# Performance work log

Measured on AMD Instinct MI355X. Metric: run time of the kernel, lower is better.

Reference implementation:

```python
import jax, jax.numpy as jnp
import numpy as np

PRIMES = [2, 3, 5, 7]  # from prime2idx {"2":0,"3":1,"5":2,"7":3}
NEG = float('-inf')


def setup_inputs() -> dict:
    B, O, T, P, L = 16384, 7, 64, 4, 7
    ks = jax.random.split(jax.random.key(0), 12)
    return {
        'program_seq': jax.random.randint(ks[0], (B, 20), 0, 7),
        'order_mask': jnp.zeros((B, O), jnp.float32),
        'tile_remain_budgets': jax.random.randint(ks[1], (B, L, P), 0, T),
        'tile_masks': jnp.zeros((B, L, P, T), jnp.float32),
        'cur_buffer_level': 1,
        'loop_ind': 2,
        'remain_buffer_size': jax.random.uniform(ks[2], (B,), jnp.float32, 1.0, 1e6),
        'tile2_max': jax.random.randint(ks[3], (B,), 32, T),
        'max_temporal_tile2': jax.random.uniform(ks[4], (B,), jnp.float32, 0.0, 10.0),
        'sp_tile2_max': jax.random.randint(ks[5], (B,), 16, 32),
        'sp_tile2_min': jax.random.randint(ks[6], (B,), 0, 8),
        'order_logit': jax.random.normal(ks[7], (B, O), jnp.float32),
        'tile_logits': jax.random.normal(ks[8], (B, P, T), jnp.float32),
        'sp_tile2_logit': jax.random.normal(ks[9], (B, T), jnp.float32),
    }


def _sample(key, score, mask):
    # categorical sample, its log-prob, and the 'more-than-one-option' mask
    action = jax.random.categorical(key, score)
    lp = jnp.take_along_axis(jax.nn.log_softmax(score, axis=-1), action[:, None], axis=1)[:, 0]
    lpm = ((mask == 0).sum(axis=-1) > 1).astype(score.dtype)
    return action, lp, lpm


def reference(program_seq, order_mask, tile_remain_budgets, tile_masks,
              cur_buffer_level, loop_ind, remain_buffer_size, tile2_max,
              max_temporal_tile2, sp_tile2_max, sp_tile2_min,
              order_logit, tile_logits, sp_tile2_logit):
    B = program_seq.shape[0]
    T = tile_masks.shape[-1]
    P = tile_logits.shape[1]
    n_levels = 3  # len(buffer_size_list)
    keys = jax.random.split(jax.random.key(1), 2 + P)
    j = jnp.arange(T)[None, :]  # [1,T] position grid for range masks

    # ---- order head ----
    order_score = order_logit + order_mask
    order_action, order_lp, order_lpm = _sample(keys[0], order_score, order_mask)

    if cur_buffer_level == n_levels:
        log_probs = jnp.zeros((B, 1 + P + 1), order_score.dtype).at[:, 0].set(order_lp)
        log_prob_masks = jnp.zeros((B, 1 + P + 1), order_score.dtype).at[:, 0].set(order_lpm)
        return order_action, None, None, log_probs, log_prob_masks

    tile2_base = tile_masks[:, loop_ind, 0]  # [B,T]

    # ---- spatial tile2: vectorized [min,max] range mask (replaces per-sample loops) ----
    sp_mask = jnp.where((j > sp_tile2_max[:, None]) | (j < sp_tile2_min[:, None]), NEG, tile2_base)
    sp_score = sp_tile2_logit + sp_mask
    sp_action, sp_lp, sp_lpm = _sample(keys[1], sp_score, sp_mask)

    # ---- temporal tile2 ----
    tile2_min = sp_action
    t2_max = jnp.minimum(tile2_max, tile2_min + max_temporal_tile2.astype(tile2_max.dtype))
    t2_mask = jnp.where((j > t2_max[:, None]) | (j < tile2_min[:, None]), NEG, tile2_base)
    t2_score = tile_logits[:, 0] + t2_mask
    tile2_action, t2_lp, t2_lpm = _sample(keys[2], t2_score, t2_mask)

    tile_actions = [tile2_action]
    sp_tile_actions = [sp_action]
    log_probs = [order_lp, t2_lp]
    log_prob_masks = [order_lpm, t2_lpm]

    tile_action = tile2_action
    rbs = remain_buffer_size
    for p in range(1, P):  # small fixed loop over primes
        rbs = rbs / jnp.power(jnp.float32(PRIMES[p - 1]), tile_action.astype(jnp.float32))
        tmax = jnp.log2(jnp.clip(rbs, 1.0)) / np.log2(PRIMES[p])
        tmax = jnp.clip(tmax.astype(jnp.int32), 0, T - 1)
        tmax = jnp.minimum(tmax, tile_remain_budgets[:, loop_ind, p].astype(jnp.int32))
        mask = jnp.where(j > tmax[:, None], NEG, tile_masks[:, loop_ind, p])
        score = tile_logits[:, p] + mask
        tile_action, lp, lpm = _sample(keys[2 + p], score, mask)
        tile_actions.append(tile_action)
        log_probs.append(lp)
        log_prob_masks.append(lpm)
        sp_tile_actions.append(jnp.zeros((B,), program_seq.dtype))

    log_probs.append(sp_lp)
    log_prob_masks.append(sp_lpm)

    return (order_action,
            jnp.stack(tile_actions, axis=1),
            jnp.stack(sp_tile_actions, axis=1),
            jnp.stack(log_probs, axis=1),
            jnp.stack(log_prob_masks, axis=1))
```

## Files before the change

### kernel.cpp

```cpp
#include <hip/hip_runtime.h>
#include <stdint.h>
#include <math.h>

__host__ __device__ static inline void tf2x32(uint32_t k0, uint32_t k1,
                                              uint32_t& x0, uint32_t& x1) {
  uint32_t ks2 = k0 ^ k1 ^ 0x1BD11BDAu;
  x0 += k0; x1 += k1;
#define TFR(r) { x0 += x1; x1 = (x1 << (r)) | (x1 >> (32 - (r))); x1 ^= x0; }
  TFR(13) TFR(15) TFR(26) TFR(6)
  x0 += k1;  x1 += ks2 + 1u;
  TFR(17) TFR(29) TFR(16) TFR(24)
  x0 += ks2; x1 += k0 + 2u;
  TFR(13) TFR(15) TFR(26) TFR(6)
  x0 += k0;  x1 += k1 + 3u;
  TFR(17) TFR(29) TFR(16) TFR(24)
  x0 += k1;  x1 += ks2 + 4u;
  TFR(13) TFR(15) TFR(26) TFR(6)
  x0 += ks2; x1 += k0 + 5u;
#undef TFR
}

struct Keys { uint32_t k[12]; };

struct SampleOut { int action; float lp; float lpm; };

template <int CTRL>
__device__ __forceinline__ float dpp_max_step(float v) {
  int o = __builtin_amdgcn_update_dpp(__float_as_int(v), __float_as_int(v),
                                      CTRL, 0xf, 0xf, false);
  return fmaxf(v, __int_as_float(o));
}
template <int CTRL>
__device__ __forceinline__ float dpp_add_step(float v) {
  int o = __builtin_amdgcn_update_dpp(0, __float_as_int(v),
                                      CTRL, 0xf, 0xf, false);
  return v + __int_as_float(o);
}
__device__ __forceinline__ float wave_max_bcast(float v) {
  v = dpp_max_step<0x111>(v);
  v = dpp_max_step<0x112>(v);
  v = dpp_max_step<0x114>(v);
  v = dpp_max_step<0x118>(v);
  v = dpp_max_step<0x142>(v);
  v = dpp_max_step<0x143>(v);
  return __int_as_float(__builtin_amdgcn_readlane(__float_as_int(v), 63));
}
__device__ __forceinline__ float wave_sum_bcast(float v) {
  v = dpp_add_step<0x111>(v);
  v = dpp_add_step<0x112>(v);
  v = dpp_add_step<0x114>(v);
  v = dpp_add_step<0x118>(v);
  v = dpp_add_step<0x142>(v);
  v = dpp_add_step<0x143>(v);
  return __int_as_float(__builtin_amdgcn_readlane(__float_as_int(v), 63));
}

__device__ static inline SampleOut sample_pre(float z, float es, float sc_full,
                                              bool lpm_pred) {
  float zmax = wave_max_bcast(z);
  unsigned long long ball = __ballot(z == zmax);
  int action = __ffsll(ball) - 1;
  float essum = wave_sum_bcast(es);
  float sa = __int_as_float(
      __builtin_amdgcn_readlane(__float_as_int(sc_full), action));
  unsigned long long mb = __ballot(lpm_pred);
  SampleOut r;
  r.action = action;
  r.lp = sa - logf(essum);
  r.lpm = (__popcll(mb) > 1) ? 1.0f : 0.0f;
  return r;
}

__device__ static inline double ipow_d(int base, int e) {
  double r = 1.0, b = (double)base;
#pragma unroll
  for (int i = 0; i < 6; ++i) {
    if (e & (1 << i)) r *= b;
    b *= b;
  }
  return r;
}

__device__ static inline float gumbel_f(uint32_t k0, uint32_t k1,
                                        uint32_t flat_idx) {
  uint32_t x0 = 0u, x1 = flat_idx;
  tf2x32(k0, k1, x0, x1);
  uint32_t bits = x0 ^ x1;
  uint32_t fb = (bits >> 9) | 0x3f800000u;
  float f = __uint_as_float(fb) - 1.0f;
  const float tinyf = 1.1754943508222875e-38f;
  float u = fmaxf(tinyf, f + tinyf);
  return -logf(-logf(u));
}

__global__ __launch_bounds__(256) void pt_kernel(
    const int*   __restrict__ loop_ind_p,
    const float* __restrict__ order_mask,
    const int*   __restrict__ tile_remain_budgets,
    const float* __restrict__ tile_masks,
    const float* __restrict__ remain_buffer_size,
    const int*   __restrict__ tile2_max,
    const float* __restrict__ max_temporal_tile2,
    const int*   __restrict__ sp_tile2_max,
    const int*   __restrict__ sp_tile2_min,
    const float* __restrict__ order_logit,
    const float* __restrict__ tile_logits,
    const float* __restrict__ sp_tile2_logit,
    float*       __restrict__ out,
    int B, int O, int T, int P, int L, Keys keys) {
  const int wave = threadIdx.x >> 6;
  const int t    = threadIdx.x & 63;
  const int b    = blockIdx.x * (blockDim.x >> 6) + wave;
  if (b >= B) return;

  const float NEGINF = -__builtin_inff();
  const int li = loop_ind_p[0];

  float g0 = gumbel_f(keys.k[0],  keys.k[1],  (uint32_t)(b * O + t));
  uint32_t fT = (uint32_t)(b * T + t);
  float g1 = gumbel_f(keys.k[2],  keys.k[3],  fT);
  float g2 = gumbel_f(keys.k[4],  keys.k[5],  fT);
  float g3 = gumbel_f(keys.k[6],  keys.k[7],  fT);
  float g4 = gumbel_f(keys.k[8],  keys.k[9],  fT);
  float g5 = gumbel_f(keys.k[10], keys.k[11], fT);

  float om  = (t < O) ? order_mask[(size_t)b * O + t] : 1.0f;
  float osc = (t < O) ? (order_logit[(size_t)b * O + t] + om) : NEGINF;

  const float* tm_row = tile_masks + ((size_t)b * L + li) * P * T;
  const float* tl_row = tile_logits + (size_t)b * P * T;
  float base0 = tm_row[t];
  float base1 = tm_row[T + t];
  float base2 = tm_row[2 * T + t];
  float base3 = tm_row[3 * T + t];

  int spmx = sp_tile2_max[b], spmn = sp_tile2_min[b];
  float spmask = (t > spmx || t < spmn) ? NEGINF : base0;
  float spsc   = sp_tile2_logit[(size_t)b * T + t] + spmask;

  float sc2f = tl_row[t]         + base0;
  float sc3f = tl_row[T + t]     + base1;
  float sc4f = tl_row[2 * T + t] + base2;
  float sc5f = tl_row[3 * T + t] + base3;
  float es2f = expf(sc2f), es3f = expf(sc3f);
  float es4f = expf(sc4f), es5f = expf(sc5f);
  float z2f = sc2f + g2, z3f = sc3f + g3, z4f = sc4f + g4, z5f = sc5f + g5;

  const int* budg = tile_remain_budgets + ((size_t)b * L + li) * P;

  SampleOut so = sample_pre(osc + g0, expf(osc), osc,
                            (t < O) && (om == 0.0f));

  SampleOut ssp = sample_pre(spsc + g1, expf(spsc), spsc, spmask == 0.0f);

  int t2min = ssp.action;
  int mt = (int)max_temporal_tile2[b];
  int t2mx = min(tile2_max[b], t2min + mt);
  bool pv2 = (t <= t2mx) && (t >= t2min);
  SampleOut st2 = sample_pre(pv2 ? z2f : NEGINF, pv2 ? es2f : 0.0f, sc2f,
                             pv2 && (base0 == 0.0f));

  const float L2P1 = 1.5849625007211562f;
  const float L2P2 = 2.321928094887362f;
  const float L2P3 = 2.807354922057604f;

  float rbs = remain_buffer_size[b];
  int   pact[3];
  float plp[3], plpm[3];

  int prev = st2.action;
  {
    rbs = (float)((double)rbs / ipow_d(2, prev));
    double v = log2(fmax((double)rbs, 1.0)) / (double)L2P1;
    int tmax = min(T - 1, max(0, (int)v));
    tmax = min(tmax, budg[1]);
    bool pv = (t <= tmax);
    SampleOut s = sample_pre(pv ? z3f : NEGINF, pv ? es3f : 0.0f, sc3f,
                             pv && (base1 == 0.0f));
    pact[0] = s.action; plp[0] = s.lp; plpm[0] = s.lpm; prev = s.action;
  }
  {
    rbs = (float)((double)rbs / ipow_d(3, prev));
    double v = log2(fmax((double)rbs, 1.0)) / (double)L2P2;
    int tmax = min(T - 1, max(0, (int)v));
    tmax = min(tmax, budg[2]);
    bool pv = (t <= tmax);
    SampleOut s = sample_pre(pv ? z4f : NEGINF, pv ? es4f : 0.0f, sc4f,
                             pv && (base2 == 0.0f));
    pact[1] = s.action; plp[1] = s.lp; plpm[1] = s.lpm; prev = s.action;
  }
  {
    rbs = (float)((double)rbs / ipow_d(5, prev));
    double v = log2(fmax((double)rbs, 1.0)) / (double)L2P3;
    int tmax = min(T - 1, max(0, (int)v));
    tmax = min(tmax, budg[3]);
    bool pv = (t <= tmax);
    SampleOut s = sample_pre(pv ? z5f : NEGINF, pv ? es5f : 0.0f, sc5f,
                             pv && (base3 == 0.0f));
    pact[2] = s.action; plp[2] = s.lp; plpm[2] = s.lpm;
  }

  if (t == 0) {
    size_t Bz = (size_t)B;
    out[b] = (float)so.action;
    float* ta = out + Bz + (size_t)b * P;
    ta[0] = (float)st2.action;
    ta[1] = (float)pact[0]; ta[2] = (float)pact[1]; ta[3] = (float)pact[2];
    float* sa = out + Bz * (1 + P) + (size_t)b * P;
    sa[0] = (float)ssp.action; sa[1] = 0.0f; sa[2] = 0.0f; sa[3] = 0.0f;
    const int NL = 6;
    float* lp = out + Bz * (1 + 2 * P) + (size_t)b * NL;
    lp[0] = so.lp; lp[1] = st2.lp;
    lp[2] = plp[0]; lp[3] = plp[1]; lp[4] = plp[2];
    lp[5] = ssp.lp;
    float* lm = out + Bz * (1 + 2 * P + NL) + (size_t)b * NL;
    lm[0] = so.lpm; lm[1] = st2.lpm;
    lm[2] = plpm[0]; lm[3] = plpm[1]; lm[4] = plpm[2];
    lm[5] = ssp.lpm;
  }
}

extern "C" void kernel_launch(void* const* d_in, const int* in_sizes, int n_in,
                              void* d_out, int out_size, void* d_ws,
                              size_t ws_size, hipStream_t stream) {
  const int B = in_sizes[6];
  const int O = in_sizes[1] / B;
  const int T = in_sizes[13] / B;
  const int P = in_sizes[12] / (B * T);
  const int L = in_sizes[2] / (B * P);

  Keys keys;
  for (int j = 0; j < 6; ++j) {
    uint32_t x0 = 0u, x1 = (uint32_t)j;
    tf2x32(0u, 1u, x0, x1);
    keys.k[2 * j]     = x0;
    keys.k[2 * j + 1] = x1;
  }

  const int wavesPerBlock = 4;
  dim3 block(wavesPerBlock * 64);
  dim3 grid((B + wavesPerBlock - 1) / wavesPerBlock);
  pt_kernel<<<grid, block, 0, stream>>>(
      (const int*)d_in[5],
      (const float*)d_in[1],
      (const int*)d_in[2],
      (const float*)d_in[3],
      (const float*)d_in[6],
      (const int*)d_in[7],
      (const float*)d_in[8],
      (const int*)d_in[9],
      (const int*)d_in[10],
      (const float*)d_in[11],
      (const float*)d_in[12],
      (const float*)d_in[13],
      (float*)d_out, B, O, T, P, L, keys);
}
```

Baseline: 214.6 us.

## Replace double log2/pow chain with constant threshold tables and ballot counting

Replaces the serial double-precision power and log2 computation of each prime's tile bound with per-lane lookups into precomputed constant tables. Each lane holds one inverse power and one threshold, and the bound is obtained by ballot and popcount. Scalar loads are hoisted ahead of the sampling chain, the action index is made wave-uniform with readfirstlane, and the per-row output stores are vectorized. This shortens the latency-bound dependent chain per row, but threshold rounding must exactly match the reference's float/double log2 truncation.

```diff
diff --git a/kernel.cpp b/kernel.cpp
--- a/kernel.cpp
+++ b/kernel.cpp
@@ -24,6 +24,37 @@
 
 struct SampleOut { int action; float lp; float lpm; };
 
+struct DTab { double v[64]; };
+
+constexpr double CEXP2(double w) {
+  long i = (long)w;
+  double f = w - (double)i;
+  double y = f * 0.69314718055994530941723212145818;
+  double term = 1.0, sum = 1.0;
+  for (int k = 1; k <= 18; ++k) { term = term * y / (double)k; sum += term; }
+  double p = 1.0;
+  for (long k = 0; k < i; ++k) p *= 2.0;
+  return sum * p;
+}
+constexpr DTab make_thresh(double l2p) {
+  DTab t{};
+  t.v[0] = 1e300;
+  for (int k = 1; k < 64; ++k) t.v[k] = CEXP2((double)k * l2p);
+  return t;
+}
+constexpr DTab make_invpw(int p) {
+  DTab t{};
+  double pw = 1.0;
+  for (int k = 0; k < 64; ++k) { t.v[k] = 1.0 / pw; pw *= (double)p; }
+  return t;
+}
+__constant__ DTab THR3 = make_thresh((double)1.5849625007211562f);
+__constant__ DTab THR5 = make_thresh((double)2.321928094887362f);
+__constant__ DTab THR7 = make_thresh((double)2.807354922057604f);
+__constant__ DTab IPW2 = make_invpw(2);
+__constant__ DTab IPW3 = make_invpw(3);
+__constant__ DTab IPW5 = make_invpw(5);
+
 template <int CTRL>
 __device__ __forceinline__ float dpp_max_step(float v) {
   int o = __builtin_amdgcn_update_dpp(__float_as_int(v), __float_as_int(v),
@@ -55,11 +86,19 @@
   return __int_as_float(__builtin_amdgcn_readlane(__float_as_int(v), 63));
 }
 
+__device__ __forceinline__ double readlane_d(double v, int lane) {
+  union { double d; int i[2]; } u, r;
+  u.d = v;
+  r.i[0] = __builtin_amdgcn_readlane(u.i[0], lane);
+  r.i[1] = __builtin_amdgcn_readlane(u.i[1], lane);
+  return r.d;
+}
+
 __device__ static inline SampleOut sample_pre(float z, float es, float sc_full,
                                               bool lpm_pred) {
   float zmax = wave_max_bcast(z);
   unsigned long long ball = __ballot(z == zmax);
-  int action = __ffsll(ball) - 1;
+  int action = __builtin_amdgcn_readfirstlane(__ffsll(ball) - 1);
   float essum = wave_sum_bcast(es);
   float sa = __int_as_float(
       __builtin_amdgcn_readlane(__float_as_int(sc_full), action));
@@ -68,16 +107,6 @@
   r.action = action;
   r.lp = sa - logf(essum);
   r.lpm = (__popcll(mb) > 1) ? 1.0f : 0.0f;
-  return r;
-}
-
-__device__ static inline double ipow_d(int base, int e) {
-  double r = 1.0, b = (double)base;
-#pragma unroll
-  for (int i = 0; i < 6; ++i) {
-    if (e & (1 << i)) r *= b;
-    b *= b;
-  }
   return r;
 }
 
@@ -116,6 +145,9 @@
   const float NEGINF = -__builtin_inff();
   const int li = loop_ind_p[0];
 
+  double thr3 = THR3.v[t], thr5 = THR5.v[t], thr7 = THR7.v[t];
+  double ipw2 = IPW2.v[t], ipw3 = IPW3.v[t], ipw5 = IPW5.v[t];
+
   float g0 = gumbel_f(keys.k[0],  keys.k[1],  (uint32_t)(b * O + t));
   uint32_t fT = (uint32_t)(b * T + t);
   float g1 = gumbel_f(keys.k[2],  keys.k[3],  fT);
@@ -147,6 +179,10 @@
   float z2f = sc2f + g2, z3f = sc3f + g3, z4f = sc4f + g4, z5f = sc5f + g5;
 
   const int* budg = tile_remain_budgets + ((size_t)b * L + li) * P;
+  int bu1 = budg[1], bu2 = budg[2], bu3 = budg[3];
+  int t2maxcap = tile2_max[b];
+  int mt = (int)max_temporal_tile2[b];
+  float rbs = remain_buffer_size[b];
 
   SampleOut so = sample_pre(osc + g0, expf(osc), osc,
                             (t < O) && (om == 0.0f));
@@ -154,46 +190,37 @@
   SampleOut ssp = sample_pre(spsc + g1, expf(spsc), spsc, spmask == 0.0f);
 
   int t2min = ssp.action;
-  int mt = (int)max_temporal_tile2[b];
-  int t2mx = min(tile2_max[b], t2min + mt);
+  int t2mx = min(t2maxcap, t2min + mt);
   bool pv2 = (t <= t2mx) && (t >= t2min);
   SampleOut st2 = sample_pre(pv2 ? z2f : NEGINF, pv2 ? es2f : 0.0f, sc2f,
                              pv2 && (base0 == 0.0f));
 
-  const float L2P1 = 1.5849625007211562f;
-  const float L2P2 = 2.321928094887362f;
-  const float L2P3 = 2.807354922057604f;
-
-  float rbs = remain_buffer_size[b];
   int   pact[3];
   float plp[3], plpm[3];
 
   int prev = st2.action;
   {
-    rbs = (float)((double)rbs / ipow_d(2, prev));
-    double v = log2(fmax((double)rbs, 1.0)) / (double)L2P1;
-    int tmax = min(T - 1, max(0, (int)v));
-    tmax = min(tmax, budg[1]);
+    rbs = (float)((double)rbs * readlane_d(ipw2, prev));
+    double x = (double)fmaxf(rbs, 1.0f);
+    int tmax = min((int)__popcll(__ballot(x >= thr3)), bu1);
     bool pv = (t <= tmax);
     SampleOut s = sample_pre(pv ? z3f : NEGINF, pv ? es3f : 0.0f, sc3f,
                              pv && (base1 == 0.0f));
     pact[0] = s.action; plp[0] = s.lp; plpm[0] = s.lpm; prev = s.action;
   }
   {
-    rbs = (float)((double)rbs / ipow_d(3, prev));
-    double v = log2(fmax((double)rbs, 1.0)) / (double)L2P2;
-    int tmax = min(T - 1, max(0, (int)v));
-    tmax = min(tmax, budg[2]);
+    rbs = (float)((double)rbs * readlane_d(ipw3, prev));
+    double x = (double)fmaxf(rbs, 1.0f);
+    int tmax = min((int)__popcll(__ballot(x >= thr5)), bu2);
     bool pv = (t <= tmax);
     SampleOut s = sample_pre(pv ? z4f : NEGINF, pv ? es4f : 0.0f, sc4f,
                              pv && (base2 == 0.0f));
     pact[1] = s.action; plp[1] = s.lp; plpm[1] = s.lpm; prev = s.action;
   }
   {
-    rbs = (float)((double)rbs / ipow_d(5, prev));
-    double v = log2(fmax((double)rbs, 1.0)) / (double)L2P3;
-    int tmax = min(T - 1, max(0, (int)v));
-    tmax = min(tmax, budg[3]);
+    rbs = (float)((double)rbs * readlane_d(ipw5, prev));
+    double x = (double)fmaxf(rbs, 1.0f);
+    int tmax = min((int)__popcll(__ballot(x >= thr7)), bu3);
     bool pv = (t <= tmax);
     SampleOut s = sample_pre(pv ? z5f : NEGINF, pv ? es5f : 0.0f, sc5f,
                              pv && (base3 == 0.0f));
@@ -203,20 +230,35 @@
   if (t == 0) {
     size_t Bz = (size_t)B;
     out[b] = (float)so.action;
-    float* ta = out + Bz + (size_t)b * P;
-    ta[0] = (float)st2.action;
-    ta[1] = (float)pact[0]; ta[2] = (float)pact[1]; ta[3] = (float)pact[2];
-    float* sa = out + Bz * (1 + P) + (size_t)b * P;
-    sa[0] = (float)ssp.action; sa[1] = 0.0f; sa[2] = 0.0f; sa[3] = 0.0f;
-    const int NL = 6;
-    float* lp = out + Bz * (1 + 2 * P) + (size_t)b * NL;
-    lp[0] = so.lp; lp[1] = st2.lp;
-    lp[2] = plp[0]; lp[3] = plp[1]; lp[4] = plp[2];
-    lp[5] = ssp.lp;
-    float* lm = out + Bz * (1 + 2 * P + NL) + (size_t)b * NL;
-    lm[0] = so.lpm; lm[1] = st2.lpm;
-    lm[2] = plpm[0]; lm[3] = plpm[1]; lm[4] = plpm[2];
-    lm[5] = ssp.lpm;
+    if (((B & 3) == 0)) {
+      float4 ta4; ta4.x = (float)st2.action; ta4.y = (float)pact[0];
+      ta4.z = (float)pact[1]; ta4.w = (float)pact[2];
+      *(float4*)(out + Bz + (size_t)b * 4) = ta4;
+      float4 sa4; sa4.x = (float)ssp.action; sa4.y = 0.0f;
+      sa4.z = 0.0f; sa4.w = 0.0f;
+      *(float4*)(out + Bz * 5 + (size_t)b * 4) = sa4;
+      float* lp = out + Bz * 9 + (size_t)b * 6;
+      float2 a, c, d;
+      a.x = so.lp;  a.y = st2.lp;  *(float2*)(lp) = a;
+      c.x = plp[0]; c.y = plp[1];  *(float2*)(lp + 2) = c;
+      d.x = plp[2]; d.y = ssp.lp;  *(float2*)(lp + 4) = d;
+      float* lm = out + Bz * 15 + (size_t)b * 6;
+      a.x = so.lpm;  a.y = st2.lpm;  *(float2*)(lm) = a;
+      c.x = plpm[0]; c.y = plpm[1];  *(float2*)(lm + 2) = c;
+      d.x = plpm[2]; d.y = ssp.lpm;  *(float2*)(lm + 4) = d;
+    } else {
+      float* ta = out + Bz + (size_t)b * 4;
+      ta[0] = (float)st2.action; ta[1] = (float)pact[0];
+      ta[2] = (float)pact[1];    ta[3] = (float)pact[2];
+      float* sa = out + Bz * 5 + (size_t)b * 4;
+      sa[0] = (float)ssp.action; sa[1] = 0.0f; sa[2] = 0.0f; sa[3] = 0.0f;
+      float* lp = out + Bz * 9 + (size_t)b * 6;
+      lp[0] = so.lp; lp[1] = st2.lp; lp[2] = plp[0];
+      lp[3] = plp[1]; lp[4] = plp[2]; lp[5] = ssp.lp;
+      float* lm = out + Bz * 15 + (size_t)b * 6;
+      lm[0] = so.lpm; lm[1] = st2.lpm; lm[2] = plpm[0];
+      lm[3] = plpm[1]; lm[4] = plpm[2]; lm[5] = ssp.lpm;
+    }
   }
 }
 
```

New measurement: 206.9 us. 3.6% less time.
